# Performance work log

Hardware: AMD Instinct MI355X
Metric: run time of the kernel (lower is better)

## Reference

```python
import jax, jax.numpy as jnp
import numpy as np

N_NODES = 20000
D = 256            # input_dim (forced by 32x16 reshape: 2*D == 512)
N_EDGES = 320000


def _init(key, shape, scale=0.02):
    return scale * jax.random.normal(key, shape, jnp.float32)


def setup_inputs() -> dict:
    key = jax.random.key(0)
    ks = jax.random.split(key, 20)
    x = jax.random.normal(ks[0], (N_NODES, D), jnp.float32)
    edge = jax.random.randint(ks[1], (N_EDGES, 2), 0, N_NODES, dtype=jnp.int64)
    params = dict(
        W_gcn=_init(ks[2], (D, 2 * D)), b_gcn=jnp.zeros((2 * D,), jnp.float32),
        conv1_w=_init(ks[3], (1, 1, 3, 3)), conv1_b=jnp.zeros((1,), jnp.float32),
        conv2_w=_init(ks[4], (1, 1, 3, 3)), conv2_b=jnp.zeros((1,), jnp.float32),
        Wc1=_init(ks[5], (2 * D, 2 * D)), bc1=jnp.zeros((2 * D,), jnp.float32),
        Wc2=_init(ks[6], (2 * D, 2 * D)), bc2=jnp.zeros((2 * D,), jnp.float32),
        Wc3=_init(ks[7], (2 * D, 2 * D)), bc3=jnp.zeros((2 * D,), jnp.float32),
        Wp1=_init(ks[8], (4 * D, 2 * D)), bp1=jnp.zeros((2 * D,), jnp.float32),
        Wp2=_init(ks[9], (2 * D, D)), bp2=jnp.zeros((D,), jnp.float32),
        Wp3=_init(ks[10], (D, D // 2)), bp3=jnp.zeros((D // 2,), jnp.float32),
        Wp4=_init(ks[11], (D // 2, 2)), bp4=jnp.zeros((2,), jnp.float32),
    )
    return dict(x=x, edge=edge, **params)


def _gcn_conv(x, edge, W, b):
    # PyG GCNConv: add self-loops, symmetric deg^-1/2 normalization, scatter-add at dst
    src, dst = edge[:, 0], edge[:, 1]
    loops = jnp.arange(N_NODES, dtype=edge.dtype)
    src = jnp.concatenate([src, loops])
    dst = jnp.concatenate([dst, loops])
    xw = x @ W                                              # [N, 2D]
    deg = jax.ops.segment_sum(jnp.ones_like(dst, jnp.float32), dst, N_NODES)
    dinv = jnp.where(deg > 0, jax.lax.rsqrt(jnp.maximum(deg, 1e-12)), 0.0)
    norm = dinv[src] * dinv[dst]                            # [E+N]
    agg = jax.ops.segment_sum(norm[:, None] * xw[src], dst, N_NODES)
    return agg + b


def reference(x, edge, W_gcn, b_gcn, conv1_w, conv1_b, conv2_w, conv2_b,
              Wc1, bc1, Wc2, bc2, Wc3, bc3,
              Wp1, bp1, Wp2, bp2, Wp3, bp3, Wp4, bp4):
    # First stage: GCNConv + ReLU, then sum readout over nodes -> [1, 2D]
    h = jax.nn.relu(_gcn_conv(x, edge, W_gcn, b_gcn))
    h = jnp.sum(h, axis=0, keepdims=True)                   # [1, 512]

    img = h.reshape(1, 1, 32, 16)
    dn = ('NCHW', 'OIHW', 'NCHW')
    c = jax.nn.relu(jax.lax.conv_general_dilated(img, conv1_w, (1, 1), 'SAME', dimension_numbers=dn) + conv1_b.reshape(1, -1, 1, 1))
    c = jax.nn.relu(jax.lax.conv_general_dilated(c, conv2_w, (1, 1), 'SAME', dimension_numbers=dn) + conv2_b.reshape(1, -1, 1, 1))
    high_conf = jax.nn.softmax(c.reshape(1, -1), axis=1)    # [1, 512]

    # Second stage, branch B: 3-layer MLP with softmax
    f = jax.nn.relu(h @ Wc1 + bc1)
    f = jax.nn.relu(f @ Wc2 + bc2)
    front = jax.nn.softmax(f @ Wc3 + bc3, axis=1)           # [1, 512]

    complete = jnp.concatenate([high_conf, front], axis=1)  # [1, 1024]

    # Predictor MLP: 1024 -> 512 -> 256 -> 128 -> 2, sigmoid
    p = jax.nn.relu(complete @ Wp1 + bp1)
    p = jax.nn.relu(p @ Wp2 + bp2)
    p = jax.nn.relu(p @ Wp3 + bp3)
    pre = jax.nn.sigmoid(p @ Wp4 + bp4)                     # [1, 2]
    return pre
```

## Files before the change

kernel.cpp:

```cpp
#include <hip/hip_runtime.h>

#define N_NODES 20000
#define N_EDGES 320000
#define DD      256
#define D2      512
#define BCAP    64

typedef short short8 __attribute__((ext_vector_type(8)));
typedef float f32x4  __attribute__((ext_vector_type(4)));
typedef float f32x2  __attribute__((ext_vector_type(2)));

__device__ __forceinline__ unsigned f2b(float f) {
    unsigned u = __float_as_uint(f);
    u = u + 0x7fffu + ((u >> 16) & 1u);
    return u >> 16;
}

__device__ __forceinline__ unsigned decode_cnt(unsigned c) {
    return (c >= 0xAAAAAAAAu) ? c - 0xAAAAAAAAu : c;
}

__global__ void k1_prep(const int* __restrict__ edge, unsigned* __restrict__ cnt,
                        int* __restrict__ csr, const float* __restrict__ x,
                        const float* __restrict__ Wg, unsigned short* __restrict__ WT,
                        unsigned* __restrict__ xf8, int* __restrict__ zbase) {
    int blk = blockIdx.x, tid = threadIdx.x;
    if (blk < 1250) {
        int e = blk * 256 + tid;
        if (e < N_EDGES) {
            int s = edge[2 * e], d = edge[2 * e + 1];
            unsigned pos = atomicAdd(&cnt[d], 1u);
            unsigned rel = decode_cnt(pos);
            if (rel < BCAP) csr[d * BCAP + rel] = s;
        }
    } else if (blk < 1282) {
        int i = (blk - 1250) * 256 + tid;
        #pragma unroll
        for (int r = 0; r < 16; r++) {
            int idx = i + r * 8192;
            int k = idx >> 9, n = idx & 511;
            WT[n * 256 + k] = (unsigned short)f2b(Wg[idx]);
        }
    } else if (blk < 6282) {
        int i = (blk - 1282) * 256 + tid;
        float4 v = ((const float4*)x)[i];
        unsigned o = 0;
        o = __builtin_amdgcn_cvt_pk_fp8_f32(v.x, v.y, o, false);
        o = __builtin_amdgcn_cvt_pk_fp8_f32(v.z, v.w, o, true);
        xf8[i] = o;
    } else {
        int i = (blk - 6282) * 256 + tid;
        zbase[i] = 0;
    }
}

__device__ __forceinline__ float dinv_of(const unsigned* cnt, int n) {
    return rsqrtf((float)(decode_cnt(cnt[n]) + 1u));
}
__device__ __forceinline__ void acc16p(f32x2* a, float w, uint4 u) {
    f32x2 wv = {w, w};
    unsigned uu[4] = {u.x, u.y, u.z, u.w};
    #pragma unroll
    for (int q = 0; q < 4; q++) {
        a[q * 2 + 0] += wv * __builtin_amdgcn_cvt_pk_f32_fp8(uu[q], false);
        a[q * 2 + 1] += wv * __builtin_amdgcn_cvt_pk_f32_fp8(uu[q], true);
    }
}

__global__ void k4_agg(const unsigned* __restrict__ cnt, const int* __restrict__ csr,
                       const unsigned char* __restrict__ xf8,
                       unsigned short* __restrict__ aggX) {
    int wid = threadIdx.x >> 6, lane = threadIdx.x & 63;
    int g = lane >> 4, l16 = lane & 15;
    int n = blockIdx.x * 4 + wid;
    f32x2 a[8];
    #pragma unroll
    for (int j = 0; j < 8; j++) a[j] = (f32x2){0.f, 0.f};
    if (n < N_NODES) {
        int deg = (int)decode_cnt(cnt[n]);
        if (deg > BCAP) deg = BCAP;
        const int* bkt = csr + n * BCAP;
        int e = 0;
        for (; e + 8 <= deg; e += 8) {
            int s0 = bkt[e + g], s1 = bkt[e + 4 + g];
            uint4 u0 = *(const uint4*)(xf8 + (size_t)s0 * DD + l16 * 16);
            uint4 u1 = *(const uint4*)(xf8 + (size_t)s1 * DD + l16 * 16);
            float w0 = dinv_of(cnt, s0), w1 = dinv_of(cnt, s1);
            acc16p(a, w0, u0); acc16p(a, w1, u1);
        }
        for (; e < deg; e += 4) {
            int idx = e + g;
            int cidx = idx < deg ? idx : deg - 1;
            int s = bkt[cidx];
            uint4 u = *(const uint4*)(xf8 + (size_t)s * DD + l16 * 16);
            float w = idx < deg ? dinv_of(cnt, s) : 0.f;
            acc16p(a, w, u);
        }
        #pragma unroll
        for (int j = 0; j < 8; j++) {
            a[j].x += __shfl_xor(a[j].x, 16, 64);
            a[j].x += __shfl_xor(a[j].x, 32, 64);
            a[j].y += __shfl_xor(a[j].y, 16, 64);
            a[j].y += __shfl_xor(a[j].y, 32, 64);
        }
        float dn = dinv_of(cnt, n), dn2 = dn * dn;
        f32x2 dv = {dn, dn}, dv2 = {dn2, dn2};
        uint4 u = *(const uint4*)(xf8 + (size_t)n * DD + l16 * 16);
        unsigned uu[4] = {u.x, u.y, u.z, u.w};
        #pragma unroll
        for (int q = 0; q < 4; q++) {
            a[q * 2 + 0] = dv * a[q * 2 + 0] + dv2 * __builtin_amdgcn_cvt_pk_f32_fp8(uu[q], false);
            a[q * 2 + 1] = dv * a[q * 2 + 1] + dv2 * __builtin_amdgcn_cvt_pk_f32_fp8(uu[q], true);
        }
    }
    if (g == 0) {
        unsigned o[8];
        #pragma unroll
        for (int j = 0; j < 8; j++) o[j] = f2b(a[j].x) | (f2b(a[j].y) << 16);
        uint4* dst = (uint4*)(aggX + (size_t)n * DD + l16 * 16);
        dst[0] = make_uint4(o[0], o[1], o[2], o[3]);
        dst[1] = make_uint4(o[4], o[5], o[6], o[7]);
    }
}

#define TN 128
#define BPAD 268
__global__ void __launch_bounds__(256, 2)
k5_gemm(const unsigned short* __restrict__ aggX, const unsigned short* __restrict__ WT,
        const float* __restrict__ bg, float* __restrict__ h) {
    __shared__ unsigned short bsh[TN * BPAD];
    __shared__ float hblk[TN];
    int tid = threadIdx.x;
    int rowblk = blockIdx.x;
    int ct = blockIdx.y;
    #pragma unroll
    for (int i = 0; i < 16; i++) {
        int c = tid + i * 256;
        int r = c >> 5;
        int kc = (c & 31) << 3;
        *(short8*)(&bsh[r * BPAD + kc]) = *(const short8*)(WT + (size_t)(ct * TN + r) * DD + kc);
    }
    if (tid < TN) hblk[tid] = 0.f;
    __syncthreads();

    int w = tid >> 6, lane = tid & 63;
    int quad = lane >> 4, l15 = lane & 15;
    int row0 = rowblk * 128 + w * 32 + l15;
    f32x4 acc[2][8];
    #pragma unroll
    for (int s = 0; s < 2; s++)
        #pragma unroll
        for (int nt = 0; nt < 8; nt++) acc[s][nt] = (f32x4){0.f, 0.f, 0.f, 0.f};
    #pragma unroll
    for (int kt = 0; kt < 8; kt++) {
        short8 a0 = *(const short8*)(aggX + (size_t)row0 * DD + kt * 32 + quad * 8);
        short8 a1 = *(const short8*)(aggX + (size_t)(row0 + 16) * DD + kt * 32 + quad * 8);
        #pragma unroll
        for (int nt = 0; nt < 8; nt++) {
            short8 b = *(const short8*)(&bsh[(nt * 16 + l15) * BPAD + kt * 32 + quad * 8]);
            acc[0][nt] = __builtin_amdgcn_mfma_f32_16x16x32_bf16(a0, b, acc[0][nt], 0, 0, 0);
            acc[1][nt] = __builtin_amdgcn_mfma_f32_16x16x32_bf16(a1, b, acc[1][nt], 0, 0, 0);
        }
    }
    #pragma unroll
    for (int s = 0; s < 2; s++) {
        int rowbase = rowblk * 128 + w * 32 + s * 16 + quad * 4;
        #pragma unroll
        for (int nt = 0; nt < 8; nt++) {
            int cl = nt * 16 + l15;
            float bias = bg[ct * TN + cl];
            float sum = 0.f;
            #pragma unroll
            for (int r = 0; r < 4; r++) {
                if (rowbase + r < N_NODES) {
                    float v = acc[s][nt][r] + bias;
                    sum += v > 0.f ? v : 0.f;
                }
            }
            sum += __shfl_xor(sum, 16, 64);
            sum += __shfl_xor(sum, 32, 64);
            if (quad == 0) atomicAdd(&hblk[cl], sum);
        }
    }
    __syncthreads();
    if (tid < TN) atomicAdd(&h[ct * TN + tid], hblk[tid]);
}

__global__ void k_mv(const float* __restrict__ in, const float* __restrict__ bias,
                     const float* __restrict__ W, float* __restrict__ out, int N, int act) {
    int c = blockIdx.y * 256 + threadIdx.x;
    int k0 = blockIdx.x * 8;
    float s = 0.f;
    #pragma unroll
    for (int kk = 0; kk < 8; kk++) {
        int k = k0 + kk;
        float v = in[k];
        if (act) { v += bias[k]; v = v > 0.f ? v : 0.f; }
        s += v * W[(size_t)k * N + c];
    }
    atomicAdd(&out[c], s);
}

__global__ void k9_mid(const float* __restrict__ h, const float* __restrict__ w1, const float* __restrict__ b1,
                       const float* __restrict__ w2, const float* __restrict__ b2,
                       const float* __restrict__ l3raw, const float* __restrict__ bc3,
                       float* __restrict__ complete) {
    __shared__ float img[512];
    __shared__ float c1s[512];
    __shared__ float red[512];
    int t = threadIdx.x;
    img[t] = h[t];
    __syncthreads();
    int y = t >> 4, x = t & 15;
    float s = 0.f;
    #pragma unroll
    for (int dy = -1; dy <= 1; dy++)
        #pragma unroll
        for (int dx = -1; dx <= 1; dx++) {
            int yy = y + dy, xc = x + dx;
            if (yy >= 0 && yy < 32 && xc >= 0 && xc < 16)
                s += w1[(dy + 1) * 3 + (dx + 1)] * img[yy * 16 + xc];
        }
    s += b1[0];
    c1s[t] = s > 0.f ? s : 0.f;
    __syncthreads();
    float s2 = 0.f;
    #pragma unroll
    for (int dy = -1; dy <= 1; dy++)
        #pragma unroll
        for (int dx = -1; dx <= 1; dx++) {
            int yy = y + dy, xc = x + dx;
            if (yy >= 0 && yy < 32 && xc >= 0 && xc < 16)
                s2 += w2[(dy + 1) * 3 + (dx + 1)] * c1s[yy * 16 + xc];
        }
    s2 += b2[0];
    float v2 = s2 > 0.f ? s2 : 0.f;
    red[t] = v2; __syncthreads();
    for (int off = 256; off > 0; off >>= 1) { if (t < off) red[t] = fmaxf(red[t], red[t + off]); __syncthreads(); }
    float m = red[0]; __syncthreads();
    float e = expf(v2 - m);
    red[t] = e; __syncthreads();
    for (int off = 256; off > 0; off >>= 1) { if (t < off) red[t] += red[t + off]; __syncthreads(); }
    complete[t] = e / red[0];
    __syncthreads();
    float z = l3raw[t] + bc3[t];
    red[t] = z; __syncthreads();
    for (int off = 256; off > 0; off >>= 1) { if (t < off) red[t] = fmaxf(red[t], red[t + off]); __syncthreads(); }
    float m2 = red[0]; __syncthreads();
    float e2 = expf(z - m2);
    red[t] = e2; __syncthreads();
    for (int off = 256; off > 0; off >>= 1) { if (t < off) red[t] += red[t + off]; __syncthreads(); }
    complete[512 + t] = e2 / red[0];
}

__global__ void k12_final(const float* __restrict__ p2raw, const float* __restrict__ bp2,
                          const float* __restrict__ Wp3, const float* __restrict__ bp3,
                          const float* __restrict__ Wp4, const float* __restrict__ bp4,
                          float* __restrict__ out) {
    __shared__ float p2s[256];
    __shared__ float p3s[128];
    int t = threadIdx.x;
    float v = p2raw[t] + bp2[t];
    p2s[t] = v > 0.f ? v : 0.f;
    __syncthreads();
    if (t < 128) {
        float s = bp3[t];
        #pragma unroll 8
        for (int k = 0; k < 256; k++) s += p2s[k] * Wp3[k * 128 + t];
        p3s[t] = s > 0.f ? s : 0.f;
    }
    __syncthreads();
    if (t < 2) {
        float s = bp4[t];
        for (int k = 0; k < 128; k++) s += p3s[k] * Wp4[k * 2 + t];
        out[t] = 1.f / (1.f + expf(-s));
    }
}

extern "C" void kernel_launch(void* const* d_in, const int* in_sizes, int n_in,
                              void* d_out, int out_size, void* d_ws, size_t ws_size,
                              hipStream_t stream) {
    const float* x    = (const float*)d_in[0];
    const int*   edge = (const int*)d_in[1];
    const float* Wg   = (const float*)d_in[2];
    const float* bg   = (const float*)d_in[3];
    const float* c1w  = (const float*)d_in[4];
    const float* c1b  = (const float*)d_in[5];
    const float* c2w  = (const float*)d_in[6];
    const float* c2b  = (const float*)d_in[7];
    const float* Wc1  = (const float*)d_in[8];
    const float* bc1  = (const float*)d_in[9];
    const float* Wc2  = (const float*)d_in[10];
    const float* bc2  = (const float*)d_in[11];
    const float* Wc3  = (const float*)d_in[12];
    const float* bc3  = (const float*)d_in[13];
    const float* Wp1  = (const float*)d_in[14];
    const float* bp1  = (const float*)d_in[15];
    const float* Wp2  = (const float*)d_in[16];
    const float* bp2  = (const float*)d_in[17];
    const float* Wp3  = (const float*)d_in[18];
    const float* bp3  = (const float*)d_in[19];
    const float* Wp4  = (const float*)d_in[20];
    const float* bp4  = (const float*)d_in[21];
    float* out = (float*)d_out;

    char* ws = (char*)d_ws;
    unsigned* cnt   = (unsigned*)(ws + 0);
    float* h        = (float*)(ws + 80000);
    float* f1raw    = (float*)(ws + 82048);
    float* f2raw    = (float*)(ws + 84096);
    float* l3raw    = (float*)(ws + 86144);
    float* p1raw    = (float*)(ws + 88192);
    float* p2raw    = (float*)(ws + 90240);
    int*   zbase    = (int*)(ws + 80000);
    float* complete = (float*)(ws + 91264);
    int*   csr      = (int*)(ws + 95360);
    unsigned short* WT   = (unsigned short*)(ws + 5215360);
    unsigned char*  xf8  = (unsigned char*)(ws + 5477504);
    unsigned short* aggX = (unsigned short*)(ws + 10597504);
    (void)ws_size; (void)in_sizes; (void)n_in; (void)out_size;

    k1_prep<<<6293, 256, 0, stream>>>(edge, cnt, csr, x, Wg, WT, (unsigned*)xf8, zbase);
    k4_agg<<<5008, 256, 0, stream>>>(cnt, csr, xf8, aggX);
    k5_gemm<<<dim3(157, 4), 256, 0, stream>>>(aggX, WT, bg, h);
    k_mv<<<dim3(64, 2), 256, 0, stream>>>(h,     nullptr, Wc1, f1raw, 512, 0);
    k_mv<<<dim3(64, 2), 256, 0, stream>>>(f1raw, bc1,     Wc2, f2raw, 512, 1);
    k_mv<<<dim3(64, 2), 256, 0, stream>>>(f2raw, bc2,     Wc3, l3raw, 512, 1);
    k9_mid<<<1, 512, 0, stream>>>(h, c1w, c1b, c2w, c2b, l3raw, bc3, complete);
    k_mv<<<dim3(128, 2), 256, 0, stream>>>(complete, nullptr, Wp1, p1raw, 512, 0);
    k_mv<<<dim3(64, 1), 256, 0, stream>>>(p1raw, bp1, Wp2, p2raw, 256, 1);
    k12_final<<<1, 256, 0, stream>>>(p2raw, bp2, Wp3, bp3, Wp4, bp4, out);
}
```

Measured before the change: 200.2 us.

## Fuse aggregation into GEMM via LDS tile and merge tail MLPs into one grid-barrier kernel

The neighbor aggregation now writes each 32-row bf16 tile into shared memory and immediately runs the MFMA GEMM plus ReLU/sum readout in the same block. This removes the aggX round trip through global memory and one launch. The seven small tail kernels become one persistent 128-block kernel that separates its stages with atomic-counter grid barriers, which removes launch overhead. The risks are weight B fragments now read straight from global/L2 for every block, much more total GEMM weight traffic, and a grid barrier that relies on all 128 blocks being co-resident.

```diff
diff --git a/kernel.cpp b/kernel.cpp
--- a/kernel.cpp
+++ b/kernel.cpp
@@ -50,10 +50,12 @@
         xf8[i] = o;
     } else {
         int i = (blk - 6282) * 256 + tid;
-        zbase[i] = 0;
-    }
-}
-
+        if (i < 2832) zbase[i] = 0;
+    }
+}
+
+#define AROWS 32
+#define AP    264
 __device__ __forceinline__ float dinv_of(const unsigned* cnt, int n) {
     return rsqrtf((float)(decode_cnt(cnt[n]) + 1u));
 }
@@ -67,213 +69,280 @@
     }
 }
 
-__global__ void k4_agg(const unsigned* __restrict__ cnt, const int* __restrict__ csr,
-                       const unsigned char* __restrict__ xf8,
-                       unsigned short* __restrict__ aggX) {
-    int wid = threadIdx.x >> 6, lane = threadIdx.x & 63;
+__global__ void __launch_bounds__(256, 2)
+kb_aggemm(const unsigned* __restrict__ cnt, const int* __restrict__ csr,
+          const unsigned char* __restrict__ xf8, const unsigned short* __restrict__ WT,
+          const float* __restrict__ bg, float* __restrict__ h) {
+    __shared__ unsigned short ash[AROWS * AP];
+    __shared__ float hblk[512];
+    int tid = threadIdx.x;
+    int w = tid >> 6, lane = tid & 63;
     int g = lane >> 4, l16 = lane & 15;
-    int n = blockIdx.x * 4 + wid;
-    f32x2 a[8];
-    #pragma unroll
-    for (int j = 0; j < 8; j++) a[j] = (f32x2){0.f, 0.f};
-    if (n < N_NODES) {
-        int deg = (int)decode_cnt(cnt[n]);
-        if (deg > BCAP) deg = BCAP;
-        const int* bkt = csr + n * BCAP;
-        int e = 0;
-        for (; e + 8 <= deg; e += 8) {
-            int s0 = bkt[e + g], s1 = bkt[e + 4 + g];
-            uint4 u0 = *(const uint4*)(xf8 + (size_t)s0 * DD + l16 * 16);
-            uint4 u1 = *(const uint4*)(xf8 + (size_t)s1 * DD + l16 * 16);
-            float w0 = dinv_of(cnt, s0), w1 = dinv_of(cnt, s1);
-            acc16p(a, w0, u0); acc16p(a, w1, u1);
-        }
-        for (; e < deg; e += 4) {
-            int idx = e + g;
-            int cidx = idx < deg ? idx : deg - 1;
-            int s = bkt[cidx];
-            uint4 u = *(const uint4*)(xf8 + (size_t)s * DD + l16 * 16);
-            float w = idx < deg ? dinv_of(cnt, s) : 0.f;
-            acc16p(a, w, u);
-        }
-        #pragma unroll
-        for (int j = 0; j < 8; j++) {
-            a[j].x += __shfl_xor(a[j].x, 16, 64);
-            a[j].x += __shfl_xor(a[j].x, 32, 64);
-            a[j].y += __shfl_xor(a[j].y, 16, 64);
-            a[j].y += __shfl_xor(a[j].y, 32, 64);
-        }
-        float dn = dinv_of(cnt, n), dn2 = dn * dn;
-        f32x2 dv = {dn, dn}, dv2 = {dn2, dn2};
-        uint4 u = *(const uint4*)(xf8 + (size_t)n * DD + l16 * 16);
-        unsigned uu[4] = {u.x, u.y, u.z, u.w};
-        #pragma unroll
-        for (int q = 0; q < 4; q++) {
-            a[q * 2 + 0] = dv * a[q * 2 + 0] + dv2 * __builtin_amdgcn_cvt_pk_f32_fp8(uu[q], false);
-            a[q * 2 + 1] = dv * a[q * 2 + 1] + dv2 * __builtin_amdgcn_cvt_pk_f32_fp8(uu[q], true);
-        }
-    }
-    if (g == 0) {
-        unsigned o[8];
-        #pragma unroll
-        for (int j = 0; j < 8; j++) o[j] = f2b(a[j].x) | (f2b(a[j].y) << 16);
-        uint4* dst = (uint4*)(aggX + (size_t)n * DD + l16 * 16);
-        dst[0] = make_uint4(o[0], o[1], o[2], o[3]);
-        dst[1] = make_uint4(o[4], o[5], o[6], o[7]);
-    }
-}
-
-#define TN 128
-#define BPAD 268
-__global__ void __launch_bounds__(256, 2)
-k5_gemm(const unsigned short* __restrict__ aggX, const unsigned short* __restrict__ WT,
-        const float* __restrict__ bg, float* __restrict__ h) {
-    __shared__ unsigned short bsh[TN * BPAD];
-    __shared__ float hblk[TN];
-    int tid = threadIdx.x;
-    int rowblk = blockIdx.x;
-    int ct = blockIdx.y;
-    #pragma unroll
-    for (int i = 0; i < 16; i++) {
-        int c = tid + i * 256;
-        int r = c >> 5;
-        int kc = (c & 31) << 3;
-        *(short8*)(&bsh[r * BPAD + kc]) = *(const short8*)(WT + (size_t)(ct * TN + r) * DD + kc);
-    }
-    if (tid < TN) hblk[tid] = 0.f;
+
+    int nbase = blockIdx.x * AROWS + w * 8;
+    for (int i = 0; i < 8; i++) {
+        int n = nbase + i;
+        f32x2 a[8];
+        #pragma unroll
+        for (int j = 0; j < 8; j++) a[j] = (f32x2){0.f, 0.f};
+        if (n < N_NODES) {
+            int deg = (int)decode_cnt(cnt[n]);
+            if (deg > BCAP) deg = BCAP;
+            const int* bkt = csr + (size_t)n * BCAP;
+            int e = 0;
+            for (; e + 8 <= deg; e += 8) {
+                int s0 = bkt[e + g], s1 = bkt[e + 4 + g];
+                uint4 u0 = *(const uint4*)(xf8 + (size_t)s0 * DD + l16 * 16);
+                uint4 u1 = *(const uint4*)(xf8 + (size_t)s1 * DD + l16 * 16);
+                float w0 = dinv_of(cnt, s0), w1 = dinv_of(cnt, s1);
+                acc16p(a, w0, u0); acc16p(a, w1, u1);
+            }
+            for (; e < deg; e += 4) {
+                int idx = e + g;
+                int cidx = idx < deg ? idx : deg - 1;
+                int s = bkt[cidx];
+                uint4 u = *(const uint4*)(xf8 + (size_t)s * DD + l16 * 16);
+                float wgt = idx < deg ? dinv_of(cnt, s) : 0.f;
+                acc16p(a, wgt, u);
+            }
+            #pragma unroll
+            for (int j = 0; j < 8; j++) {
+                a[j].x += __shfl_xor(a[j].x, 16, 64);
+                a[j].x += __shfl_xor(a[j].x, 32, 64);
+                a[j].y += __shfl_xor(a[j].y, 16, 64);
+                a[j].y += __shfl_xor(a[j].y, 32, 64);
+            }
+            float dn = dinv_of(cnt, n), dn2 = dn * dn;
+            f32x2 dv = {dn, dn}, dv2 = {dn2, dn2};
+            uint4 u = *(const uint4*)(xf8 + (size_t)n * DD + l16 * 16);
+            unsigned uu[4] = {u.x, u.y, u.z, u.w};
+            #pragma unroll
+            for (int q = 0; q < 4; q++) {
+                a[q * 2 + 0] = dv * a[q * 2 + 0] + dv2 * __builtin_amdgcn_cvt_pk_f32_fp8(uu[q], false);
+                a[q * 2 + 1] = dv * a[q * 2 + 1] + dv2 * __builtin_amdgcn_cvt_pk_f32_fp8(uu[q], true);
+            }
+        }
+        if (g == 0) {
+            unsigned o[8];
+            #pragma unroll
+            for (int j = 0; j < 8; j++) o[j] = f2b(a[j].x) | (f2b(a[j].y) << 16);
+            int rl = w * 8 + i;
+            uint4* dst = (uint4*)&ash[(size_t)rl * AP + l16 * 16];
+            dst[0] = make_uint4(o[0], o[1], o[2], o[3]);
+            dst[1] = make_uint4(o[4], o[5], o[6], o[7]);
+        }
+    }
     __syncthreads();
 
-    int w = tid >> 6, lane = tid & 63;
     int quad = lane >> 4, l15 = lane & 15;
-    int row0 = rowblk * 128 + w * 32 + l15;
+    int colbase = w * 128;
     f32x4 acc[2][8];
     #pragma unroll
     for (int s = 0; s < 2; s++)
         #pragma unroll
         for (int nt = 0; nt < 8; nt++) acc[s][nt] = (f32x4){0.f, 0.f, 0.f, 0.f};
+    const unsigned short* wbase = WT + (size_t)colbase * 256;
     #pragma unroll
     for (int kt = 0; kt < 8; kt++) {
-        short8 a0 = *(const short8*)(aggX + (size_t)row0 * DD + kt * 32 + quad * 8);
-        short8 a1 = *(const short8*)(aggX + (size_t)(row0 + 16) * DD + kt * 32 + quad * 8);
+        short8 av0 = *(const short8*)&ash[(size_t)l15 * AP + kt * 32 + quad * 8];
+        short8 av1 = *(const short8*)&ash[(size_t)(16 + l15) * AP + kt * 32 + quad * 8];
+        short8 bb[8];
+        #pragma unroll
+        for (int nt = 0; nt < 8; nt++)
+            bb[nt] = *(const short8*)(wbase + (size_t)(nt * 16 + l15) * 256 + kt * 32 + quad * 8);
         #pragma unroll
         for (int nt = 0; nt < 8; nt++) {
-            short8 b = *(const short8*)(&bsh[(nt * 16 + l15) * BPAD + kt * 32 + quad * 8]);
-            acc[0][nt] = __builtin_amdgcn_mfma_f32_16x16x32_bf16(a0, b, acc[0][nt], 0, 0, 0);
-            acc[1][nt] = __builtin_amdgcn_mfma_f32_16x16x32_bf16(a1, b, acc[1][nt], 0, 0, 0);
-        }
-    }
-    #pragma unroll
-    for (int s = 0; s < 2; s++) {
-        int rowbase = rowblk * 128 + w * 32 + s * 16 + quad * 4;
-        #pragma unroll
-        for (int nt = 0; nt < 8; nt++) {
-            int cl = nt * 16 + l15;
-            float bias = bg[ct * TN + cl];
-            float sum = 0.f;
+            acc[0][nt] = __builtin_amdgcn_mfma_f32_16x16x32_bf16(av0, bb[nt], acc[0][nt], 0, 0, 0);
+            acc[1][nt] = __builtin_amdgcn_mfma_f32_16x16x32_bf16(av1, bb[nt], acc[1][nt], 0, 0, 0);
+        }
+    }
+    #pragma unroll
+    for (int nt = 0; nt < 8; nt++) {
+        int cl = colbase + nt * 16 + l15;
+        float bias = bg[cl];
+        float csum = 0.f;
+        #pragma unroll
+        for (int s = 0; s < 2; s++) {
+            int rowbase = blockIdx.x * AROWS + s * 16 + quad * 4;
             #pragma unroll
             for (int r = 0; r < 4; r++) {
                 if (rowbase + r < N_NODES) {
                     float v = acc[s][nt][r] + bias;
-                    sum += v > 0.f ? v : 0.f;
+                    csum += v > 0.f ? v : 0.f;
                 }
             }
-            sum += __shfl_xor(sum, 16, 64);
-            sum += __shfl_xor(sum, 32, 64);
-            if (quad == 0) atomicAdd(&hblk[cl], sum);
-        }
+        }
+        csum += __shfl_xor(csum, 16, 64);
+        csum += __shfl_xor(csum, 32, 64);
+        if (quad == 0) hblk[cl] = csum;
     }
     __syncthreads();
-    if (tid < TN) atomicAdd(&h[ct * TN + tid], hblk[tid]);
-}
-
-__global__ void k_mv(const float* __restrict__ in, const float* __restrict__ bias,
-                     const float* __restrict__ W, float* __restrict__ out, int N, int act) {
-    int c = blockIdx.y * 256 + threadIdx.x;
-    int k0 = blockIdx.x * 8;
+    atomicAdd(&h[tid], hblk[tid]);
+    atomicAdd(&h[tid + 256], hblk[tid + 256]);
+}
+
+#define KC_NB 128u
+__device__ __forceinline__ void gbar(unsigned* bar, int idx) {
+    __syncthreads();
+    if (threadIdx.x == 0) {
+        __threadfence();
+        atomicAdd(&bar[idx], 1u);
+        while (__hip_atomic_load(&bar[idx], __ATOMIC_ACQUIRE, __HIP_MEMORY_SCOPE_AGENT) < KC_NB) {
+            __builtin_amdgcn_s_sleep(1);
+        }
+    }
+    __syncthreads();
+}
+
+__device__ __forceinline__ float conv3(const float* im, const float* wgt, int idx) {
+    int y = idx >> 4, x = idx & 15;
     float s = 0.f;
     #pragma unroll
-    for (int kk = 0; kk < 8; kk++) {
-        int k = k0 + kk;
-        float v = in[k];
-        if (act) { v += bias[k]; v = v > 0.f ? v : 0.f; }
-        s += v * W[(size_t)k * N + c];
-    }
-    atomicAdd(&out[c], s);
-}
-
-__global__ void k9_mid(const float* __restrict__ h, const float* __restrict__ w1, const float* __restrict__ b1,
-                       const float* __restrict__ w2, const float* __restrict__ b2,
-                       const float* __restrict__ l3raw, const float* __restrict__ bc3,
-                       float* __restrict__ complete) {
-    __shared__ float img[512];
-    __shared__ float c1s[512];
-    __shared__ float red[512];
-    int t = threadIdx.x;
-    img[t] = h[t];
-    __syncthreads();
-    int y = t >> 4, x = t & 15;
-    float s = 0.f;
-    #pragma unroll
     for (int dy = -1; dy <= 1; dy++)
         #pragma unroll
         for (int dx = -1; dx <= 1; dx++) {
-            int yy = y + dy, xc = x + dx;
-            if (yy >= 0 && yy < 32 && xc >= 0 && xc < 16)
-                s += w1[(dy + 1) * 3 + (dx + 1)] * img[yy * 16 + xc];
-        }
-    s += b1[0];
-    c1s[t] = s > 0.f ? s : 0.f;
-    __syncthreads();
-    float s2 = 0.f;
-    #pragma unroll
-    for (int dy = -1; dy <= 1; dy++)
-        #pragma unroll
-        for (int dx = -1; dx <= 1; dx++) {
-            int yy = y + dy, xc = x + dx;
-            if (yy >= 0 && yy < 32 && xc >= 0 && xc < 16)
-                s2 += w2[(dy + 1) * 3 + (dx + 1)] * c1s[yy * 16 + xc];
-        }
-    s2 += b2[0];
-    float v2 = s2 > 0.f ? s2 : 0.f;
-    red[t] = v2; __syncthreads();
-    for (int off = 256; off > 0; off >>= 1) { if (t < off) red[t] = fmaxf(red[t], red[t + off]); __syncthreads(); }
-    float m = red[0]; __syncthreads();
-    float e = expf(v2 - m);
-    red[t] = e; __syncthreads();
-    for (int off = 256; off > 0; off >>= 1) { if (t < off) red[t] += red[t + off]; __syncthreads(); }
-    complete[t] = e / red[0];
-    __syncthreads();
-    float z = l3raw[t] + bc3[t];
-    red[t] = z; __syncthreads();
-    for (int off = 256; off > 0; off >>= 1) { if (t < off) red[t] = fmaxf(red[t], red[t + off]); __syncthreads(); }
-    float m2 = red[0]; __syncthreads();
-    float e2 = expf(z - m2);
-    red[t] = e2; __syncthreads();
-    for (int off = 256; off > 0; off >>= 1) { if (t < off) red[t] += red[t + off]; __syncthreads(); }
-    complete[512 + t] = e2 / red[0];
-}
-
-__global__ void k12_final(const float* __restrict__ p2raw, const float* __restrict__ bp2,
-                          const float* __restrict__ Wp3, const float* __restrict__ bp3,
-                          const float* __restrict__ Wp4, const float* __restrict__ bp4,
-                          float* __restrict__ out) {
-    __shared__ float p2s[256];
-    __shared__ float p3s[128];
-    int t = threadIdx.x;
-    float v = p2raw[t] + bp2[t];
-    p2s[t] = v > 0.f ? v : 0.f;
-    __syncthreads();
-    if (t < 128) {
-        float s = bp3[t];
-        #pragma unroll 8
-        for (int k = 0; k < 256; k++) s += p2s[k] * Wp3[k * 128 + t];
-        p3s[t] = s > 0.f ? s : 0.f;
-    }
-    __syncthreads();
-    if (t < 2) {
-        float s = bp4[t];
-        for (int k = 0; k < 128; k++) s += p3s[k] * Wp4[k * 2 + t];
-        out[t] = 1.f / (1.f + expf(-s));
+            int yy = y + dy, xx = x + dx;
+            if (yy >= 0 && yy < 32 && xx >= 0 && xx < 16)
+                s += wgt[(dy + 1) * 3 + (dx + 1)] * im[yy * 16 + xx];
+        }
+    return s;
+}
+
+__global__ void __launch_bounds__(256)
+kc_tail(const float* __restrict__ h,
+        const float* __restrict__ Wc1, const float* __restrict__ bc1,
+        const float* __restrict__ Wc2, const float* __restrict__ bc2,
+        const float* __restrict__ Wc3, const float* __restrict__ bc3,
+        const float* __restrict__ c1w, const float* __restrict__ c1b,
+        const float* __restrict__ c2w, const float* __restrict__ c2b,
+        const float* __restrict__ Wp1, const float* __restrict__ bp1,
+        const float* __restrict__ Wp2, const float* __restrict__ bp2,
+        const float* __restrict__ Wp3, const float* __restrict__ bp3,
+        const float* __restrict__ Wp4, const float* __restrict__ bp4,
+        float* __restrict__ f1raw, float* __restrict__ f2raw, float* __restrict__ l3raw,
+        float* __restrict__ complete, float* __restrict__ p1raw, float* __restrict__ p2raw,
+        float* __restrict__ out, unsigned* __restrict__ bar) {
+    __shared__ float img[512], c1s[512], red[256];
+    __shared__ float p2s[256], p3s[128];
+    int b = blockIdx.x, t = threadIdx.x;
+
+    if (b < 64) {
+        int k0 = b * 8;
+        float s0 = 0.f, s1 = 0.f;
+        #pragma unroll
+        for (int kk = 0; kk < 8; kk++) {
+            float v = h[k0 + kk];
+            s0 += v * Wc1[(k0 + kk) * 512 + t];
+            s1 += v * Wc1[(k0 + kk) * 512 + t + 256];
+        }
+        atomicAdd(&f1raw[t], s0);
+        atomicAdd(&f1raw[t + 256], s1);
+    }
+    gbar(bar, 0);
+
+    if (b < 64) {
+        int k0 = b * 8;
+        float s0 = 0.f, s1 = 0.f;
+        #pragma unroll
+        for (int kk = 0; kk < 8; kk++) {
+            float v = f1raw[k0 + kk] + bc1[k0 + kk];
+            v = v > 0.f ? v : 0.f;
+            s0 += v * Wc2[(k0 + kk) * 512 + t];
+            s1 += v * Wc2[(k0 + kk) * 512 + t + 256];
+        }
+        atomicAdd(&f2raw[t], s0);
+        atomicAdd(&f2raw[t + 256], s1);
+    }
+    gbar(bar, 1);
+
+    if (b < 64) {
+        int k0 = b * 8;
+        float s0 = 0.f, s1 = 0.f;
+        #pragma unroll
+        for (int kk = 0; kk < 8; kk++) {
+            float v = f2raw[k0 + kk] + bc2[k0 + kk];
+            v = v > 0.f ? v : 0.f;
+            s0 += v * Wc3[(k0 + kk) * 512 + t];
+            s1 += v * Wc3[(k0 + kk) * 512 + t + 256];
+        }
+        atomicAdd(&l3raw[t], s0);
+        atomicAdd(&l3raw[t + 256], s1);
+    }
+    gbar(bar, 2);
+
+    if (b == 0) {
+        img[t] = h[t]; img[t + 256] = h[t + 256];
+        __syncthreads();
+        float r0 = conv3(img, c1w, t) + c1b[0];       r0 = r0 > 0.f ? r0 : 0.f;
+        float r1 = conv3(img, c1w, t + 256) + c1b[0]; r1 = r1 > 0.f ? r1 : 0.f;
+        c1s[t] = r0; c1s[t + 256] = r1;
+        __syncthreads();
+        float v0 = conv3(c1s, c2w, t) + c2b[0];       v0 = v0 > 0.f ? v0 : 0.f;
+        float v1 = conv3(c1s, c2w, t + 256) + c2b[0]; v1 = v1 > 0.f ? v1 : 0.f;
+        red[t] = fmaxf(v0, v1); __syncthreads();
+        for (int off = 128; off > 0; off >>= 1) { if (t < off) red[t] = fmaxf(red[t], red[t + off]); __syncthreads(); }
+        float m = red[0]; __syncthreads();
+        float e0 = expf(v0 - m), e1 = expf(v1 - m);
+        red[t] = e0 + e1; __syncthreads();
+        for (int off = 128; off > 0; off >>= 1) { if (t < off) red[t] += red[t + off]; __syncthreads(); }
+        float inv = 1.f / red[0];
+        complete[t] = e0 * inv; complete[t + 256] = e1 * inv;
+        __syncthreads();
+        float z0 = l3raw[t] + bc3[t], z1 = l3raw[t + 256] + bc3[t + 256];
+        red[t] = fmaxf(z0, z1); __syncthreads();
+        for (int off = 128; off > 0; off >>= 1) { if (t < off) red[t] = fmaxf(red[t], red[t + off]); __syncthreads(); }
+        float m2 = red[0]; __syncthreads();
+        float e2 = expf(z0 - m2), e3 = expf(z1 - m2);
+        red[t] = e2 + e3; __syncthreads();
+        for (int off = 128; off > 0; off >>= 1) { if (t < off) red[t] += red[t + off]; __syncthreads(); }
+        float inv2 = 1.f / red[0];
+        complete[512 + t] = e2 * inv2; complete[768 + t] = e3 * inv2;
+    }
+    gbar(bar, 3);
+
+    {
+        int k0 = b * 8;
+        float s0 = 0.f, s1 = 0.f;
+        #pragma unroll
+        for (int kk = 0; kk < 8; kk++) {
+            float v = complete[k0 + kk];
+            s0 += v * Wp1[(k0 + kk) * 512 + t];
+            s1 += v * Wp1[(k0 + kk) * 512 + t + 256];
+        }
+        atomicAdd(&p1raw[t], s0);
+        atomicAdd(&p1raw[t + 256], s1);
+    }
+    gbar(bar, 4);
+
+    if (b < 64) {
+        int k0 = b * 8;
+        float s = 0.f;
+        #pragma unroll
+        for (int kk = 0; kk < 8; kk++) {
+            float v = p1raw[k0 + kk] + bp1[k0 + kk];
+            v = v > 0.f ? v : 0.f;
+            s += v * Wp2[(k0 + kk) * 256 + t];
+        }
+        atomicAdd(&p2raw[t], s);
+    }
+    gbar(bar, 5);
+
+    if (b == 0) {
+        float v = p2raw[t] + bp2[t];
+        p2s[t] = v > 0.f ? v : 0.f;
+        __syncthreads();
+        if (t < 128) {
+            float s = bp3[t];
+            #pragma unroll 8
+            for (int k = 0; k < 256; k++) s += p2s[k] * Wp3[k * 128 + t];
+            p3s[t] = s > 0.f ? s : 0.f;
+        }
+        __syncthreads();
+        if (t < 2) {
+            float s = bp4[t];
+            for (int k = 0; k < 128; k++) s += p3s[k] * Wp4[k * 2 + t];
+            out[t] = 1.f / (1.f + expf(-s));
+        }
     }
 }
 
@@ -312,22 +381,19 @@
     float* l3raw    = (float*)(ws + 86144);
     float* p1raw    = (float*)(ws + 88192);
     float* p2raw    = (float*)(ws + 90240);
+    unsigned* bar   = (unsigned*)(ws + 91264);
     int*   zbase    = (int*)(ws + 80000);
-    float* complete = (float*)(ws + 91264);
-    int*   csr      = (int*)(ws + 95360);
-    unsigned short* WT   = (unsigned short*)(ws + 5215360);
-    unsigned char*  xf8  = (unsigned char*)(ws + 5477504);
-    unsigned short* aggX = (unsigned short*)(ws + 10597504);
+    float* complete = (float*)(ws + 91328);
+    int*   csr      = (int*)(ws + 95424);
+    unsigned short* WT   = (unsigned short*)(ws + 5215424);
+    unsigned char*  xf8  = (unsigned char*)(ws + 5477568);
     (void)ws_size; (void)in_sizes; (void)n_in; (void)out_size;
 
-    k1_prep<<<6293, 256, 0, stream>>>(edge, cnt, csr, x, Wg, WT, (unsigned*)xf8, zbase);
-    k4_agg<<<5008, 256, 0, stream>>>(cnt, csr, xf8, aggX);
-    k5_gemm<<<dim3(157, 4), 256, 0, stream>>>(aggX, WT, bg, h);
-    k_mv<<<dim3(64, 2), 256, 0, stream>>>(h,     nullptr, Wc1, f1raw, 512, 0);
-    k_mv<<<dim3(64, 2), 256, 0, stream>>>(f1raw, bc1,     Wc2, f2raw, 512, 1);
-    k_mv<<<dim3(64, 2), 256, 0, stream>>>(f2raw, bc2,     Wc3, l3raw, 512, 1);
-    k9_mid<<<1, 512, 0, stream>>>(h, c1w, c1b, c2w, c2b, l3raw, bc3, complete);
-    k_mv<<<dim3(128, 2), 256, 0, stream>>>(complete, nullptr, Wp1, p1raw, 512, 0);
-    k_mv<<<dim3(64, 1), 256, 0, stream>>>(p1raw, bp1, Wp2, p2raw, 256, 1);
-    k12_final<<<1, 256, 0, stream>>>(p2raw, bp2, Wp3, bp3, Wp4, bp4, out);
-}
+    k1_prep<<<6294, 256, 0, stream>>>(edge, cnt, csr, x, Wg, WT, (unsigned*)xf8, zbase);
+    kb_aggemm<<<625, 256, 0, stream>>>(cnt, csr, xf8, WT, bg, h);
+    kc_tail<<<128, 256, 0, stream>>>(h, Wc1, bc1, Wc2, bc2, Wc3, bc3,
+                                     c1w, c1b, c2w, c2b,
+                                     Wp1, bp1, Wp2, bp2, Wp3, bp3, Wp4, bp4,
+                                     f1raw, f2raw, l3raw, complete, p1raw, p2raw,
+                                     out, bar);
+}
```

Measured after the change: 240.7 us. 1.2x slower.

## Fuse tail MLPs and conv into one single-block kernel with bf16-packed weights

Applied to the files above, without the earlier changes.

Replaces the six matrix-vector kernels, the conv/softmax kernel and the final kernel with one 512-thread block that runs the whole tail in shared memory. The tail weights are converted to bf16 and packed in pairs during the prep kernel so the fused block reads half the bytes. This removes many launches and the atomic-accumulate intermediates. The trade-off is that a single block does all the matvecs serially on one CU, and weight precision drops to bf16.

```diff
diff --git a/kernel.cpp b/kernel.cpp
--- a/kernel.cpp
+++ b/kernel.cpp
@@ -20,10 +20,32 @@
     return (c >= 0xAAAAAAAAu) ? c - 0xAAAAAAAAu : c;
 }
 
+__device__ __forceinline__ void packW(const float* __restrict__ src, unsigned* __restrict__ dst,
+                                      int i, int logn) {
+    int N = 1 << logn;
+    int c = i & (N - 1);
+    int kp = i >> logn;
+    const float* r0 = src + ((size_t)kp << (logn + 1)) + c;
+    float4 a = *(const float4*)r0;
+    float4 b = *(const float4*)(r0 + N);
+    uint4 o;
+    o.x = f2b(a.x) | (f2b(b.x) << 16);
+    o.y = f2b(a.y) | (f2b(b.y) << 16);
+    o.z = f2b(a.z) | (f2b(b.z) << 16);
+    o.w = f2b(a.w) | (f2b(b.w) << 16);
+    *(uint4*)(dst + i) = o;
+}
+
 __global__ void k1_prep(const int* __restrict__ edge, unsigned* __restrict__ cnt,
                         int* __restrict__ csr, const float* __restrict__ x,
                         const float* __restrict__ Wg, unsigned short* __restrict__ WT,
-                        unsigned* __restrict__ xf8, int* __restrict__ zbase) {
+                        unsigned* __restrict__ xf8, int* __restrict__ hz,
+                        const float* __restrict__ Wc1, const float* __restrict__ Wc2,
+                        const float* __restrict__ Wc3, const float* __restrict__ Wp1,
+                        const float* __restrict__ Wp2, const float* __restrict__ Wp3,
+                        unsigned* __restrict__ Wc1p, unsigned* __restrict__ Wc2p,
+                        unsigned* __restrict__ Wc3p, unsigned* __restrict__ Wp1p,
+                        unsigned* __restrict__ Wp2p, unsigned* __restrict__ Wp3p) {
     int blk = blockIdx.x, tid = threadIdx.x;
     if (blk < 1250) {
         int e = blk * 256 + tid;
@@ -48,10 +70,15 @@
         o = __builtin_amdgcn_cvt_pk_fp8_f32(v.x, v.y, o, false);
         o = __builtin_amdgcn_cvt_pk_fp8_f32(v.z, v.w, o, true);
         xf8[i] = o;
-    } else {
+    } else if (blk < 6284) {
         int i = (blk - 6282) * 256 + tid;
-        zbase[i] = 0;
-    }
+        if (i < 512) hz[i] = 0;
+    } else if (blk < 6412) { packW(Wc1, Wc1p, ((blk - 6284) * 256 + tid) * 4, 9); }
+    else if (blk < 6540) { packW(Wc2, Wc2p, ((blk - 6412) * 256 + tid) * 4, 9); }
+    else if (blk < 6668) { packW(Wc3, Wc3p, ((blk - 6540) * 256 + tid) * 4, 9); }
+    else if (blk < 6924) { packW(Wp1, Wp1p, ((blk - 6668) * 256 + tid) * 4, 9); }
+    else if (blk < 6988) { packW(Wp2, Wp2p, ((blk - 6924) * 256 + tid) * 4, 8); }
+    else                 { packW(Wp3, Wp3p, ((blk - 6988) * 256 + tid) * 4, 7); }
 }
 
 __device__ __forceinline__ float dinv_of(const unsigned* cnt, int n) {
@@ -186,93 +213,117 @@
     if (tid < TN) atomicAdd(&h[ct * TN + tid], hblk[tid]);
 }
 
-__global__ void k_mv(const float* __restrict__ in, const float* __restrict__ bias,
-                     const float* __restrict__ W, float* __restrict__ out, int N, int act) {
-    int c = blockIdx.y * 256 + threadIdx.x;
-    int k0 = blockIdx.x * 8;
+__device__ __forceinline__ float mv_pk(const float* in, const unsigned* __restrict__ Wp,
+                                       int Kh, int N, int c) {
+    float a0 = 0.f, a1 = 0.f;
+    const float2* in2 = (const float2*)in;
+    #pragma unroll 4
+    for (int kp = 0; kp < Kh; kp += 2) {
+        unsigned u0 = Wp[kp * N + c];
+        unsigned u1 = Wp[(kp + 1) * N + c];
+        float2 x0 = in2[kp], x1 = in2[kp + 1];
+        a0 += x0.x * __uint_as_float(u0 << 16) + x0.y * __uint_as_float(u0 & 0xffff0000u);
+        a1 += x1.x * __uint_as_float(u1 << 16) + x1.y * __uint_as_float(u1 & 0xffff0000u);
+    }
+    return a0 + a1;
+}
+
+__device__ __forceinline__ float conv3(const float* im, const float* wgt, int idx) {
+    int y = idx >> 4, x = idx & 15;
     float s = 0.f;
     #pragma unroll
-    for (int kk = 0; kk < 8; kk++) {
-        int k = k0 + kk;
-        float v = in[k];
-        if (act) { v += bias[k]; v = v > 0.f ? v : 0.f; }
-        s += v * W[(size_t)k * N + c];
-    }
-    atomicAdd(&out[c], s);
-}
-
-__global__ void k9_mid(const float* __restrict__ h, const float* __restrict__ w1, const float* __restrict__ b1,
-                       const float* __restrict__ w2, const float* __restrict__ b2,
-                       const float* __restrict__ l3raw, const float* __restrict__ bc3,
-                       float* __restrict__ complete) {
-    __shared__ float img[512];
-    __shared__ float c1s[512];
+    for (int dy = -1; dy <= 1; dy++)
+        #pragma unroll
+        for (int dx = -1; dx <= 1; dx++) {
+            int yy = y + dy, xx = x + dx;
+            if (yy >= 0 && yy < 32 && xx >= 0 && xx < 16)
+                s += wgt[(dy + 1) * 3 + (dx + 1)] * im[yy * 16 + xx];
+        }
+    return s;
+}
+
+__global__ void __launch_bounds__(512)
+kc_tail(const float* __restrict__ h,
+        const float* __restrict__ c1w, const float* __restrict__ c1b,
+        const float* __restrict__ c2w, const float* __restrict__ c2b,
+        const float* __restrict__ bc1, const float* __restrict__ bc2, const float* __restrict__ bc3,
+        const unsigned* __restrict__ Wc1p, const unsigned* __restrict__ Wc2p,
+        const unsigned* __restrict__ Wc3p, const unsigned* __restrict__ Wp1p,
+        const unsigned* __restrict__ Wp2p, const unsigned* __restrict__ Wp3p,
+        const float* __restrict__ bp1, const float* __restrict__ bp2, const float* __restrict__ bp3,
+        const float* __restrict__ Wp4, const float* __restrict__ bp4,
+        float* __restrict__ out) {
+    __shared__ float bufA[1024];
+    __shared__ float bufB[512];
+    __shared__ float comp[1024];
     __shared__ float red[512];
     int t = threadIdx.x;
-    img[t] = h[t];
-    __syncthreads();
-    int y = t >> 4, x = t & 15;
-    float s = 0.f;
-    #pragma unroll
-    for (int dy = -1; dy <= 1; dy++)
-        #pragma unroll
-        for (int dx = -1; dx <= 1; dx++) {
-            int yy = y + dy, xc = x + dx;
-            if (yy >= 0 && yy < 32 && xc >= 0 && xc < 16)
-                s += w1[(dy + 1) * 3 + (dx + 1)] * img[yy * 16 + xc];
-        }
-    s += b1[0];
-    c1s[t] = s > 0.f ? s : 0.f;
-    __syncthreads();
-    float s2 = 0.f;
-    #pragma unroll
-    for (int dy = -1; dy <= 1; dy++)
-        #pragma unroll
-        for (int dx = -1; dx <= 1; dx++) {
-            int yy = y + dy, xc = x + dx;
-            if (yy >= 0 && yy < 32 && xc >= 0 && xc < 16)
-                s2 += w2[(dy + 1) * 3 + (dx + 1)] * c1s[yy * 16 + xc];
-        }
-    s2 += b2[0];
-    float v2 = s2 > 0.f ? s2 : 0.f;
-    red[t] = v2; __syncthreads();
-    for (int off = 256; off > 0; off >>= 1) { if (t < off) red[t] = fmaxf(red[t], red[t + off]); __syncthreads(); }
-    float m = red[0]; __syncthreads();
-    float e = expf(v2 - m);
-    red[t] = e; __syncthreads();
-    for (int off = 256; off > 0; off >>= 1) { if (t < off) red[t] += red[t + off]; __syncthreads(); }
-    complete[t] = e / red[0];
-    __syncthreads();
-    float z = l3raw[t] + bc3[t];
-    red[t] = z; __syncthreads();
-    for (int off = 256; off > 0; off >>= 1) { if (t < off) red[t] = fmaxf(red[t], red[t + off]); __syncthreads(); }
-    float m2 = red[0]; __syncthreads();
-    float e2 = expf(z - m2);
-    red[t] = e2; __syncthreads();
-    for (int off = 256; off > 0; off >>= 1) { if (t < off) red[t] += red[t + off]; __syncthreads(); }
-    complete[512 + t] = e2 / red[0];
-}
-
-__global__ void k12_final(const float* __restrict__ p2raw, const float* __restrict__ bp2,
-                          const float* __restrict__ Wp3, const float* __restrict__ bp3,
-                          const float* __restrict__ Wp4, const float* __restrict__ bp4,
-                          float* __restrict__ out) {
-    __shared__ float p2s[256];
-    __shared__ float p3s[128];
-    int t = threadIdx.x;
-    float v = p2raw[t] + bp2[t];
-    p2s[t] = v > 0.f ? v : 0.f;
+
+    bufA[t >= 512 ? 0 : t] = h[t >= 512 ? 0 : t];
+    __syncthreads();
+
+    {
+        float v = conv3(bufA, c1w, t) + c1b[0];
+        bufB[t] = v > 0.f ? v : 0.f;
+    }
+    __syncthreads();
+    {
+        float v = conv3(bufB, c2w, t) + c2b[0];
+        v = v > 0.f ? v : 0.f;
+        red[t] = v; __syncthreads();
+        for (int off = 256; off > 0; off >>= 1) { if (t < off) red[t] = fmaxf(red[t], red[t + off]); __syncthreads(); }
+        float m = red[0]; __syncthreads();
+        float e = expf(v - m);
+        red[t] = e; __syncthreads();
+        for (int off = 256; off > 0; off >>= 1) { if (t < off) red[t] += red[t + off]; __syncthreads(); }
+        comp[t] = e / red[0];
+    }
+    __syncthreads();
+
+    {
+        float v = mv_pk(bufA, Wc1p, 256, 512, t) + bc1[t];
+        __syncthreads();
+        bufB[t] = v > 0.f ? v : 0.f;
+    }
+    __syncthreads();
+    {
+        float v = mv_pk(bufB, Wc2p, 256, 512, t) + bc2[t];
+        __syncthreads();
+        bufA[t] = v > 0.f ? v : 0.f;
+    }
+    __syncthreads();
+    {
+        float z = mv_pk(bufA, Wc3p, 256, 512, t) + bc3[t];
+        red[t] = z; __syncthreads();
+        for (int off = 256; off > 0; off >>= 1) { if (t < off) red[t] = fmaxf(red[t], red[t + off]); __syncthreads(); }
+        float m = red[0]; __syncthreads();
+        float e = expf(z - m);
+        red[t] = e; __syncthreads();
+        for (int off = 256; off > 0; off >>= 1) { if (t < off) red[t] += red[t + off]; __syncthreads(); }
+        comp[512 + t] = e / red[0];
+    }
+    __syncthreads();
+
+    {
+        float v = mv_pk(comp, Wp1p, 512, 512, t) + bp1[t];
+        __syncthreads();
+        bufA[t] = v > 0.f ? v : 0.f;
+    }
+    __syncthreads();
+    if (t < 256) {
+        float v = mv_pk(bufA, Wp2p, 256, 256, t) + bp2[t];
+        bufB[t] = v > 0.f ? v : 0.f;
+    }
     __syncthreads();
     if (t < 128) {
-        float s = bp3[t];
-        #pragma unroll 8
-        for (int k = 0; k < 256; k++) s += p2s[k] * Wp3[k * 128 + t];
-        p3s[t] = s > 0.f ? s : 0.f;
+        float v = mv_pk(bufB, Wp3p, 128, 128, t) + bp3[t];
+        red[t] = v > 0.f ? v : 0.f;
     }
     __syncthreads();
     if (t < 2) {
         float s = bp4[t];
-        for (int k = 0; k < 128; k++) s += p3s[k] * Wp4[k * 2 + t];
+        #pragma unroll 8
+        for (int k = 0; k < 128; k++) s += red[k] * Wp4[k * 2 + t];
         out[t] = 1.f / (1.f + expf(-s));
     }
 }
@@ -307,27 +358,24 @@
     char* ws = (char*)d_ws;
     unsigned* cnt   = (unsigned*)(ws + 0);
     float* h        = (float*)(ws + 80000);
-    float* f1raw    = (float*)(ws + 82048);
-    float* f2raw    = (float*)(ws + 84096);
-    float* l3raw    = (float*)(ws + 86144);
-    float* p1raw    = (float*)(ws + 88192);
-    float* p2raw    = (float*)(ws + 90240);
-    int*   zbase    = (int*)(ws + 80000);
-    float* complete = (float*)(ws + 91264);
-    int*   csr      = (int*)(ws + 95360);
-    unsigned short* WT   = (unsigned short*)(ws + 5215360);
-    unsigned char*  xf8  = (unsigned char*)(ws + 5477504);
-    unsigned short* aggX = (unsigned short*)(ws + 10597504);
+    int*   csr      = (int*)(ws + 82048);
+    unsigned short* WT   = (unsigned short*)(ws + 5202048);
+    unsigned char*  xf8  = (unsigned char*)(ws + 5464192);
+    unsigned short* aggX = (unsigned short*)(ws + 10584192);
+    unsigned* Wc1p  = (unsigned*)(ws + 20873344);
+    unsigned* Wc2p  = (unsigned*)(ws + 21397632);
+    unsigned* Wc3p  = (unsigned*)(ws + 21921920);
+    unsigned* Wp1p  = (unsigned*)(ws + 22446208);
+    unsigned* Wp2p  = (unsigned*)(ws + 23494784);
+    unsigned* Wp3p  = (unsigned*)(ws + 23756928);
     (void)ws_size; (void)in_sizes; (void)n_in; (void)out_size;
 
-    k1_prep<<<6293, 256, 0, stream>>>(edge, cnt, csr, x, Wg, WT, (unsigned*)xf8, zbase);
+    k1_prep<<<7004, 256, 0, stream>>>(edge, cnt, csr, x, Wg, WT, (unsigned*)xf8, (int*)h,
+                                      Wc1, Wc2, Wc3, Wp1, Wp2, Wp3,
+                                      Wc1p, Wc2p, Wc3p, Wp1p, Wp2p, Wp3p);
     k4_agg<<<5008, 256, 0, stream>>>(cnt, csr, xf8, aggX);
     k5_gemm<<<dim3(157, 4), 256, 0, stream>>>(aggX, WT, bg, h);
-    k_mv<<<dim3(64, 2), 256, 0, stream>>>(h,     nullptr, Wc1, f1raw, 512, 0);
-    k_mv<<<dim3(64, 2), 256, 0, stream>>>(f1raw, bc1,     Wc2, f2raw, 512, 1);
-    k_mv<<<dim3(64, 2), 256, 0, stream>>>(f2raw, bc2,     Wc3, l3raw, 512, 1);
-    k9_mid<<<1, 512, 0, stream>>>(h, c1w, c1b, c2w, c2b, l3raw, bc3, complete);
-    k_mv<<<dim3(128, 2), 256, 0, stream>>>(complete, nullptr, Wp1, p1raw, 512, 0);
-    k_mv<<<dim3(64, 1), 256, 0, stream>>>(p1raw, bp1, Wp2, p2raw, 256, 1);
-    k12_final<<<1, 256, 0, stream>>>(p2raw, bp2, Wp3, bp3, Wp4, bp4, out);
-}
+    kc_tail<<<1, 512, 0, stream>>>(h, c1w, c1b, c2w, c2b, bc1, bc2, bc3,
+                                   Wc1p, Wc2p, Wc3p, Wp1p, Wp2p, Wp3p,
+                                   bp1, bp2, bp3, Wp4, bp4, out);
+}
```

Measured after the change: 255.0 us. 1.27x slower.
